# Performance work log

Hardware: AMD Instinct MI355X
Metric: run time of the kernel (lower is better)

The kernel has to match this reference:

```python
import jax, jax.numpy as jnp
import numpy as np

D_MODEL = 1024
NUM_HEADS = 16
EPS = 1e-5


def _layernorm(x, gamma, beta):
    mu = jnp.mean(x, axis=-1, keepdims=True)
    var = jnp.mean(jnp.square(x - mu), axis=-1, keepdims=True)
    return (x - mu) * jax.lax.rsqrt(var + EPS) * gamma + beta


def setup_inputs() -> dict:
    key = jax.random.key(0)
    ks = jax.random.split(key, 8)
    B, S, D = 4, 2048, D_MODEL
    xav = (6.0 / (D + D)) ** 0.5  # xavier_uniform bound for square D x D
    inp = {
        "q": jax.random.normal(ks[0], (B, S, D), dtype=jnp.float32),
        "k": jax.random.normal(ks[1], (B, S, D), dtype=jnp.float32),
        "v": jax.random.normal(ks[2], (B, S, D), dtype=jnp.float32),
        "Wq": jax.random.uniform(ks[3], (D, D), jnp.float32, -xav, xav),
        "Wk": jax.random.uniform(ks[4], (D, D), jnp.float32, -xav, xav),
        "Wv": jax.random.uniform(ks[5], (D, D), jnp.float32, -xav, xav),
        "Wo": jax.random.uniform(ks[6], (D, D), jnp.float32, -xav, xav),
        "bo": jnp.zeros((D,), jnp.float32),
        "q_gamma": jnp.ones((D,), jnp.float32),
        "q_beta": jnp.zeros((D,), jnp.float32),
        "k_gamma": jnp.ones((D,), jnp.float32),
        "k_beta": jnp.zeros((D,), jnp.float32),
    }
    return inp


def reference(q, k, v, Wq, Wk, Wv, Wo, bo, q_gamma, q_beta, k_gamma, k_beta):
    B, S, D = q.shape
    H = NUM_HEADS
    scale = 1.0 / (D ** 0.5)  # NOTE: 1/sqrt(d_model), as in the source
    qp = _layernorm(q @ Wq, q_gamma, q_beta)  # LN over full d_model, pre-split
    kp = _layernorm(k @ Wk, k_gamma, k_beta)
    vp = v @ Wv
    qh = qp.reshape(B, S, H, D // H)  # [B,S,H,hd]
    kh = kp.reshape(B, S, H, D // H)
    vh = vp.reshape(B, S, H, D // H)
    attn = jnp.einsum("bqhd,bkhd->bhqk", qh, kh) * scale
    attn = jax.nn.softmax(attn, axis=-1)
    x = jnp.einsum("bhqk,bkhd->bqhd", attn, vh).reshape(B, S, D)
    return x @ Wo + bo
```

## Files before the change

kernel.cpp:

```cpp
#include <hip/hip_runtime.h>
#include <hip/hip_bf16.h>

typedef unsigned short u16;
typedef __attribute__((ext_vector_type(8))) short bf16x8;
typedef __attribute__((ext_vector_type(4))) float f32x4;
typedef __attribute__((ext_vector_type(16))) float f32x16;
typedef __attribute__((ext_vector_type(4))) unsigned short u16x4;
typedef __attribute__((ext_vector_type(4))) unsigned int u32x4;
typedef __attribute__((ext_vector_type(2))) int i32x2;

__device__ __forceinline__ u16 f2b(float f) {
    __hip_bfloat16 h = __float2bfloat16(f);
    u16 r; __builtin_memcpy(&r, &h, 2); return r;
}
__device__ __forceinline__ float bf2f(u16 u) {
    return __uint_as_float(((unsigned)u) << 16);
}
__device__ __forceinline__ void gload16(const void* g, void* l) {
    __builtin_amdgcn_global_load_lds(
        (const __attribute__((address_space(1))) unsigned int*)g,
        (__attribute__((address_space(3))) unsigned int*)l, 16, 0, 0);
}
__device__ __forceinline__ float fexp2(float x) {
    return __builtin_amdgcn_exp2f(x);
}
__device__ __forceinline__ unsigned cvtpk(float lo, float hi) {
    unsigned d;
    asm("v_cvt_pk_bf16_f32 %0, %1, %2" : "=v"(d) : "v"(lo), "v"(hi));
    return d;
}
__device__ __forceinline__ bf16x8 mk_pa(float a0, float a1, float a2, float a3,
                                        float b0, float b1, float b2, float b3) {
    int A0 = (int)cvtpk(a0, a1), A1 = (int)cvtpk(a2, a3);
    int B0 = (int)cvtpk(b0, b1), B1 = (int)cvtpk(b2, b3);
    i32x2 r0 = __builtin_amdgcn_permlane32_swap(A0, B0, false, false);
    i32x2 r1 = __builtin_amdgcn_permlane32_swap(A1, B1, false, false);
    u32x4 fw = { (unsigned)r0[0], (unsigned)r1[0], (unsigned)r0[1], (unsigned)r1[1] };
    return __builtin_bit_cast(bf16x8, fw);
}

__global__ __launch_bounds__(256)
void wt_kernel(const float* __restrict__ Wq, const float* __restrict__ Wk,
               const float* __restrict__ Wv, const float* __restrict__ Wo,
               u16* __restrict__ Wt) {
    const float* W = blockIdx.z == 0 ? Wq : blockIdx.z == 1 ? Wk : blockIdx.z == 2 ? Wv : Wo;
    u16* Out = Wt + (size_t)blockIdx.z * (1024 * 1024);
    __shared__ float T[64][65];
    const int t = threadIdx.x;
    const int r0 = blockIdx.y * 64, c0 = blockIdx.x * 64;
#pragma unroll
    for (int e = 0; e < 4; ++e) {
        int row = e * 16 + (t >> 4), c4 = (t & 15) * 4;
        f32x4 v = *(const f32x4*)(W + (r0 + row) * 1024 + c0 + c4);
        T[row][c4] = v[0]; T[row][c4 + 1] = v[1]; T[row][c4 + 2] = v[2]; T[row][c4 + 3] = v[3];
    }
    __syncthreads();
#pragma unroll
    for (int e = 0; e < 4; ++e) {
        int orow = e * 16 + (t >> 4), oc4 = (t & 15) * 4;
        u16x4 pk = { f2b(T[oc4][orow]), f2b(T[oc4 + 1][orow]),
                     f2b(T[oc4 + 2][orow]), f2b(T[oc4 + 3][orow]) };
        *(u16x4*)(Out + (c0 + orow) * 1024 + r0 + oc4) = pk;
    }
}

template <int AF32, int BIAS>
__device__ __forceinline__ void gemm_body(const void* __restrict__ Av,
                                          const u16* __restrict__ Bt,
                                          u16* __restrict__ Cb, float* __restrict__ Cf,
                                          const float* __restrict__ bias,
                                          u16* As, u16* Bs, int bx, int by) {
    constexpr int K = 1024;
    const int tid = threadIdx.x;
    const int lane = tid & 63, w = tid >> 6;
    const int wr = w >> 1, wc = w & 1;
    const int c = lane & 15, g = lane >> 4;
    const int m0 = by * 128, n0 = bx * 128;
    const int sr = lane >> 3, sc = (lane & 7) * 8;
    const float* Af = (const float*)Av;
    const u16* Ab = (const u16*)Av;
    f32x4 acc[4][4] = {};
    for (int kt = 0; kt < 16; ++kt) {
        const int k0 = kt * 64;
        if (AF32) {
#pragma unroll
            for (int i = 0; i < 8; ++i) {
                int idx = i * 256 + tid;
                int row = idx >> 4, c4 = (idx & 15) * 4;
                f32x4 v = *(const f32x4*)(Af + (size_t)(m0 + row) * K + k0 + c4);
                u16x4 pk = { f2b(v[0]), f2b(v[1]), f2b(v[2]), f2b(v[3]) };
                *(u16x4*)&As[row * 64 + c4] = pk;
            }
        } else {
#pragma unroll
            for (int i = 0; i < 4; ++i) {
                int row = 32 * w + 8 * i;
                gload16(Ab + (size_t)(m0 + row + sr) * K + k0 + sc, &As[row * 64]);
            }
        }
#pragma unroll
        for (int i = 0; i < 4; ++i) {
            int row = 32 * w + 8 * i;
            gload16(Bt + (size_t)(n0 + row + sr) * K + k0 + sc, &Bs[row * 64]);
        }
        __syncthreads();
#pragma unroll
        for (int kk = 0; kk < 2; ++kk) {
            bf16x8 af[4], bfr[4];
#pragma unroll
            for (int m = 0; m < 4; ++m)
                af[m] = *(const bf16x8*)&As[(wr * 64 + m * 16 + c) * 64 + kk * 32 + 8 * g];
#pragma unroll
            for (int n = 0; n < 4; ++n)
                bfr[n] = *(const bf16x8*)&Bs[(wc * 64 + n * 16 + c) * 64 + kk * 32 + 8 * g];
#pragma unroll
            for (int m = 0; m < 4; ++m)
#pragma unroll
                for (int n = 0; n < 4; ++n)
                    acc[m][n] = __builtin_amdgcn_mfma_f32_16x16x32_bf16(af[m], bfr[n], acc[m][n], 0, 0, 0);
        }
        __syncthreads();
    }
#pragma unroll
    for (int n = 0; n < 4; ++n) {
        int col = n0 + wc * 64 + n * 16 + c;
        float bv = BIAS ? bias[col] : 0.0f;
#pragma unroll
        for (int m = 0; m < 4; ++m) {
            int row0 = m0 + wr * 64 + m * 16 + 4 * g;
#pragma unroll
            for (int r = 0; r < 4; ++r) {
                if (BIAS) Cf[(row0 + r) * 1024 + col] = acc[m][n][r] + bv;
                else      Cb[(row0 + r) * 1024 + col] = f2b(acc[m][n][r]);
            }
        }
    }
}

__global__ __launch_bounds__(256)
void gemm_kernel_f(const u16* __restrict__ Ab, const u16* __restrict__ Bt,
                   float* __restrict__ Cf, const float* __restrict__ bias) {
    __shared__ u16 As[128 * 64];
    __shared__ u16 Bs[128 * 64];
    const int B = blockIdx.x;
    const int bx = (B >> 3) & 7;
    const int by = (B & 7) + 8 * (B >> 6);
    gemm_body<0, 1>(Ab, Bt, nullptr, Cf, bias, As, Bs, bx, by);
}

__global__ __launch_bounds__(256)
void gemm3_kernel(const float* __restrict__ q, const float* __restrict__ k,
                  const float* __restrict__ v, const u16* __restrict__ Wt,
                  u16* __restrict__ C3) {
    __shared__ u16 As[128 * 64];
    __shared__ u16 Bs[128 * 64];
    const int B = blockIdx.x;
    const int bx = (B >> 3) & 7;
    const int p = (B & 7) + 8 * (B >> 6);
    const int by = p & 63;
    const int z = p >> 6;
    const float* Af = z == 0 ? q : z == 1 ? k : v;
    gemm_body<1, 0>((const void*)Af, Wt + (size_t)z * 1048576,
                    C3 + (size_t)z * 8388608, nullptr, nullptr, As, Bs, bx, by);
}

__global__ __launch_bounds__(256)
void gemm1_kernel(const float* __restrict__ Af, const u16* __restrict__ Bt,
                  u16* __restrict__ Cb) {
    __shared__ u16 As[128 * 64];
    __shared__ u16 Bs[128 * 64];
    const int B = blockIdx.x;
    const int bx = (B >> 3) & 7;
    const int by = (B & 7) + 8 * (B >> 6);
    gemm_body<1, 0>((const void*)Af, Bt, Cb, nullptr, nullptr, As, Bs, bx, by);
}

__device__ __forceinline__ void ln_body(const u16* __restrict__ P,
                                        const float* __restrict__ gamma,
                                        const float* __restrict__ beta,
                                        float mul, u16* __restrict__ Out) {
    const int row = blockIdx.x;
    const int tid = threadIdx.x;
    const int lane = tid & 63, w = tid >> 6;
    u16x4 xr = *(const u16x4*)(P + row * 1024 + tid * 4);
    float x0 = bf2f(xr[0]), x1 = bf2f(xr[1]), x2 = bf2f(xr[2]), x3 = bf2f(xr[3]);
    float s = x0 + x1 + x2 + x3;
    float sq = x0 * x0 + x1 * x1 + x2 * x2 + x3 * x3;
#pragma unroll
    for (int m = 1; m < 64; m <<= 1) { s += __shfl_xor(s, m); sq += __shfl_xor(sq, m); }
    __shared__ float red[8];
    if (lane == 0) { red[w] = s; red[4 + w] = sq; }
    __syncthreads();
    float st = red[0] + red[1] + red[2] + red[3];
    float sqt = red[4] + red[5] + red[6] + red[7];
    float mu = st * (1.0f / 1024.0f);
    float var = sqt * (1.0f / 1024.0f) - mu * mu;
    float rs = rsqrtf(var + 1e-5f);
    f32x4 gm = *(const f32x4*)(gamma + tid * 4);
    f32x4 bt = *(const f32x4*)(beta + tid * 4);
    float xs[4] = {x0, x1, x2, x3};
    u16x4 pk;
#pragma unroll
    for (int j = 0; j < 4; ++j)
        pk[j] = f2b(((xs[j] - mu) * rs * gm[j] + bt[j]) * mul);
    const int b = row >> 11, sI = row & 2047;
    const int col = tid * 4, hh = col >> 6, d = col & 63;
    *(u16x4*)(Out + (((b * 16 + hh) * 2048 + sI) << 6) + d) = pk;
}

__global__ __launch_bounds__(256)
void ln_kernel(const u16* __restrict__ P, const float* __restrict__ gamma,
               const float* __restrict__ beta, float mul, u16* __restrict__ Out) {
    ln_body(P, gamma, beta, mul, Out);
}

__global__ __launch_bounds__(256)
void ln2_kernel(const u16* __restrict__ P3,
                const float* __restrict__ qg, const float* __restrict__ qb,
                const float* __restrict__ kg, const float* __restrict__ kb,
                u16* __restrict__ Qa, u16* __restrict__ Ka, float mulq) {
    const int z = blockIdx.z;
    ln_body(P3 + (size_t)z * 8388608, z == 0 ? qg : kg, z == 0 ? qb : kb,
            z == 0 ? mulq : 1.0f, z == 0 ? Qa : Ka);
}

__global__ __launch_bounds__(256)
void vt_kernel(const u16* __restrict__ P, u16* __restrict__ Vt) {
    __shared__ u16 T[64][72];
    const int t = threadIdx.x;
    const int bh = blockIdx.y, s0 = blockIdx.x * 64;
    const int b = bh >> 4, h = bh & 15;
#pragma unroll
    for (int e = 0; e < 4; ++e) {
        int row = e * 16 + (t >> 4), c4 = (t & 15) * 4;
        u16x4 v = *(const u16x4*)(P + (b * 2048 + s0 + row) * 1024 + h * 64 + c4);
        *(u16x4*)&T[row][c4] = v;
    }
    __syncthreads();
#pragma unroll
    for (int e = 0; e < 4; ++e) {
        int dd = e * 16 + (t >> 4), s4 = (t & 15) * 4;
        u16x4 pk = { T[s4][dd], T[s4 + 1][dd], T[s4 + 2][dd], T[s4 + 3][dd] };
        *(u16x4*)(Vt + ((size_t)bh * 64 + dd) * 2048 + s0 + s4) = pk;
    }
}

__global__ __launch_bounds__(256, 4)
void attn_kernel(const u16* __restrict__ Qa, const u16* __restrict__ Ka,
                 const u16* __restrict__ Vt, u16* __restrict__ Xa) {
    __shared__ u16 Ks[2][4096];
    __shared__ u16 Vs[2][4096];
    const int tid = threadIdx.x;
    const int lane = tid & 63, w = tid >> 6;
    const int col = lane & 31, h = lane >> 5;
    const int bid = blockIdx.x;
    const int bh = (bid & 7) * 8 + ((bid >> 3) & 7);
    const int q0 = (bid >> 6) * 128;
    const int b = bh >> 4, hd = bh & 15;
    const int qb = q0 + w * 32;
    const int sw = (col & 7) << 4;

    const u16* qptr = Qa + ((size_t)bh * 2048 + qb + col) * 64;
    bf16x8 qf[4];
#pragma unroll
    for (int s = 0; s < 4; ++s)
        qf[s] = *(const bf16x8*)(qptr + 16 * s + 8 * h);

    const int sr = lane >> 3;
    const int scg = ((lane & 7) ^ sr) * 8;
    const u16* kA = Ka + ((size_t)bh * 2048 + sr) * 64 + scg;
    const u16* vA = Vt + ((size_t)bh * 64 + sr) * 2048 + scg;

    f32x16 o0 = {}, o1 = {};
    float li = 0.f;

#pragma unroll
    for (int j = 0; j < 2; ++j) {
        const int m = 2 * w + j;
        gload16(kA + (size_t)(8 * m) * 64, &Ks[0][8 * m * 64]);
        gload16(vA + (size_t)(8 * m) * 2048, &Vs[0][8 * m * 64]);
    }
    __syncthreads();

    int cur = 0;
    for (int t = 0; t < 32; ++t) {
        const int tn = (t + 1) & 31;
#pragma unroll
        for (int j = 0; j < 2; ++j) {
            const int m = 2 * w + j;
            gload16(kA + (size_t)(tn * 64 + 8 * m) * 64, &Ks[cur ^ 1][8 * m * 64]);
            gload16(vA + (size_t)(8 * m) * 2048 + tn * 64, &Vs[cur ^ 1][8 * m * 64]);
        }

        const char* kbase = (const char*)&Ks[cur][0];
        f32x16 sacc0 = {}, sacc1 = {};
        __builtin_amdgcn_s_setprio(1);
#pragma unroll
        for (int s = 0; s < 4; ++s) {
            bf16x8 kf0 = *(const bf16x8*)(kbase + (col) * 128       + ((32 * s + 16 * h) ^ sw));
            bf16x8 kf1 = *(const bf16x8*)(kbase + (32 + col) * 128  + ((32 * s + 16 * h) ^ sw));
            sacc0 = __builtin_amdgcn_mfma_f32_32x32x16_bf16(kf0, qf[s], sacc0, 0, 0, 0);
            sacc1 = __builtin_amdgcn_mfma_f32_32x32x16_bf16(kf1, qf[s], sacc1, 0, 0, 0);
        }
        __builtin_amdgcn_s_setprio(0);

        f32x16 p0, p1;
#pragma unroll
        for (int r = 0; r < 16; ++r) { p0[r] = fexp2(sacc0[r]); }
#pragma unroll
        for (int r = 0; r < 16; ++r) { p1[r] = fexp2(sacc1[r]); }
#pragma unroll
        for (int r = 0; r < 16; ++r) { li += p0[r] + p1[r]; }

        bf16x8 pa0 = mk_pa(p0[0], p0[1], p0[2], p0[3], p0[4], p0[5], p0[6], p0[7]);
        bf16x8 pa1 = mk_pa(p0[8], p0[9], p0[10], p0[11], p0[12], p0[13], p0[14], p0[15]);
        bf16x8 pa2 = mk_pa(p1[0], p1[1], p1[2], p1[3], p1[4], p1[5], p1[6], p1[7]);
        bf16x8 pa3 = mk_pa(p1[8], p1[9], p1[10], p1[11], p1[12], p1[13], p1[14], p1[15]);

        const char* vb = (const char*)&Vs[cur][0];
        __builtin_amdgcn_s_setprio(1);
#pragma unroll
        for (int sg = 0; sg < 4; ++sg) {
            bf16x8 pf = sg == 0 ? pa0 : sg == 1 ? pa1 : sg == 2 ? pa2 : pa3;
            const int cb = (32 * sg + 16 * h) ^ sw;
            bf16x8 vf0 = *(const bf16x8*)(vb + (col) * 128      + cb);
            bf16x8 vf1 = *(const bf16x8*)(vb + (32 + col) * 128 + cb);
            o0 = __builtin_amdgcn_mfma_f32_32x32x16_bf16(pf, vf0, o0, 0, 0, 0);
            o1 = __builtin_amdgcn_mfma_f32_32x32x16_bf16(pf, vf1, o1, 0, 0, 0);
        }
        __builtin_amdgcn_s_setprio(0);

        __syncthreads();
        cur ^= 1;
    }

    li += __shfl_xor(li, 32);
    float inv = 1.0f / li;
#pragma unroll
    for (int reg = 0; reg < 16; ++reg) {
        const int crow = (reg & 3) + 8 * (reg >> 2) + 4 * h;
        float ivr = __shfl(inv, crow);
        const int row = qb + crow;
        u16* xp = Xa + ((size_t)b * 2048 + row) * 1024 + hd * 64;
        xp[col] = f2b(o0[reg] * ivr);
        xp[32 + col] = f2b(o1[reg] * ivr);
    }
}

extern "C" void kernel_launch(void* const* d_in, const int* in_sizes, int n_in,
                              void* d_out, int out_size, void* d_ws, size_t ws_size,
                              hipStream_t stream) {
    const float* q   = (const float*)d_in[0];
    const float* k   = (const float*)d_in[1];
    const float* v   = (const float*)d_in[2];
    const float* Wq  = (const float*)d_in[3];
    const float* Wk  = (const float*)d_in[4];
    const float* Wv  = (const float*)d_in[5];
    const float* Wo  = (const float*)d_in[6];
    const float* bo  = (const float*)d_in[7];
    const float* qg  = (const float*)d_in[8];
    const float* qbt = (const float*)d_in[9];
    const float* kg  = (const float*)d_in[10];
    const float* kbt = (const float*)d_in[11];

    char* ws = (char*)d_ws;
    const float MUL_Q = 0.04508422002778f;

    if (ws_size >= 109051904ULL) {
        u16* Wt  = (u16*)(ws);
        u16* Qa  = (u16*)(ws + 8388608);
        u16* Ka  = (u16*)(ws + 25165824);
        u16* Vt  = (u16*)(ws + 41943040);
        u16* Pb3 = (u16*)(ws + 58720256);
        u16* Xa  = Pb3;

        wt_kernel<<<dim3(16, 16, 4), 256, 0, stream>>>(Wq, Wk, Wv, Wo, Wt);
        gemm3_kernel<<<1536, 256, 0, stream>>>(q, k, v, Wt, Pb3);
        ln2_kernel<<<dim3(8192, 1, 2), 256, 0, stream>>>(Pb3, qg, qbt, kg, kbt, Qa, Ka, MUL_Q);
        vt_kernel<<<dim3(32, 64), 256, 0, stream>>>(Pb3 + 2 * 8388608, Vt);
        attn_kernel<<<1024, 256, 0, stream>>>(Qa, Ka, Vt, Xa);
        gemm_kernel_f<<<512, 256, 0, stream>>>((const u16*)Xa, Wt + 3145728, (float*)d_out, bo);
    } else {
        u16* Wt = (u16*)(ws);
        u16* Pb = (u16*)(ws + 8388608);
        u16* Qa = (u16*)(ws + 25165824);
        u16* Ka = (u16*)(ws + 41943040);
        u16* Vt = (u16*)(ws + 58720256);
        u16* Xa = Pb;

        wt_kernel<<<dim3(16, 16, 4), 256, 0, stream>>>(Wq, Wk, Wv, Wo, Wt);
        gemm1_kernel<<<512, 256, 0, stream>>>(q, Wt, Pb);
        ln_kernel<<<8192, 256, 0, stream>>>(Pb, qg, qbt, MUL_Q, Qa);
        gemm1_kernel<<<512, 256, 0, stream>>>(k, Wt + 1048576, Pb);
        ln_kernel<<<8192, 256, 0, stream>>>(Pb, kg, kbt, 1.0f, Ka);
        gemm1_kernel<<<512, 256, 0, stream>>>(v, Wt + 2097152, Pb);
        vt_kernel<<<dim3(32, 64), 256, 0, stream>>>(Pb, Vt);
        attn_kernel<<<1024, 256, 0, stream>>>(Qa, Ka, Vt, Xa);
        gemm_kernel_f<<<512, 256, 0, stream>>>((const u16*)Xa, Wt + 3145728, (float*)d_out, bo);
    }
}
```

Before: 234.4 us.

## Prefetch fp32 A tiles into registers two steps ahead in projection GEMM

Adds a dedicated fp32-input GEMM body that loads the next-next A tile into registers while the current tile is consumed by MFMAs, then converts and stores to LDS after the barrier. The goal is to hide global load latency of fp32 activations that previously stalled each k-step. It costs 32 extra VGPRs for the register staging, which may reduce occupancy. The bf16 path is simplified to a single template parameter.

```diff
diff --git a/kernel.cpp b/kernel.cpp
--- a/kernel.cpp
+++ b/kernel.cpp
@@ -64,8 +64,8 @@
     }
 }
 
-template <int AF32, int BIAS>
-__device__ __forceinline__ void gemm_body(const void* __restrict__ Av,
+template <int BIAS>
+__device__ __forceinline__ void gemm_body(const u16* __restrict__ Ab,
                                           const u16* __restrict__ Bt,
                                           u16* __restrict__ Cb, float* __restrict__ Cf,
                                           const float* __restrict__ bias,
@@ -77,30 +77,13 @@
     const int c = lane & 15, g = lane >> 4;
     const int m0 = by * 128, n0 = bx * 128;
     const int sr = lane >> 3, sc = (lane & 7) * 8;
-    const float* Af = (const float*)Av;
-    const u16* Ab = (const u16*)Av;
     f32x4 acc[4][4] = {};
     for (int kt = 0; kt < 16; ++kt) {
         const int k0 = kt * 64;
-        if (AF32) {
-#pragma unroll
-            for (int i = 0; i < 8; ++i) {
-                int idx = i * 256 + tid;
-                int row = idx >> 4, c4 = (idx & 15) * 4;
-                f32x4 v = *(const f32x4*)(Af + (size_t)(m0 + row) * K + k0 + c4);
-                u16x4 pk = { f2b(v[0]), f2b(v[1]), f2b(v[2]), f2b(v[3]) };
-                *(u16x4*)&As[row * 64 + c4] = pk;
-            }
-        } else {
-#pragma unroll
-            for (int i = 0; i < 4; ++i) {
-                int row = 32 * w + 8 * i;
-                gload16(Ab + (size_t)(m0 + row + sr) * K + k0 + sc, &As[row * 64]);
-            }
-        }
 #pragma unroll
         for (int i = 0; i < 4; ++i) {
             int row = 32 * w + 8 * i;
+            gload16(Ab + (size_t)(m0 + row + sr) * K + k0 + sc, &As[row * 64]);
             gload16(Bt + (size_t)(n0 + row + sr) * K + k0 + sc, &Bs[row * 64]);
         }
         __syncthreads();
@@ -133,6 +116,91 @@
                 if (BIAS) Cf[(row0 + r) * 1024 + col] = acc[m][n][r] + bv;
                 else      Cb[(row0 + r) * 1024 + col] = f2b(acc[m][n][r]);
             }
+        }
+    }
+}
+
+__device__ __forceinline__ void gemm_body_f32(const float* __restrict__ Af,
+                                              const u16* __restrict__ Bt,
+                                              u16* __restrict__ Cb,
+                                              u16* As, u16* Bs, int bx, int by) {
+    constexpr int K = 1024;
+    const int tid = threadIdx.x;
+    const int lane = tid & 63, w = tid >> 6;
+    const int wr = w >> 1, wc = w & 1;
+    const int c = lane & 15, g = lane >> 4;
+    const int m0 = by * 128, n0 = bx * 128;
+    const int sr = lane >> 3, sc = (lane & 7) * 8;
+    const int arow = tid >> 4, ac4 = (tid & 15) * 4;
+    const float* aBase = Af + (size_t)(m0 + arow) * K + ac4;
+    f32x4 acc[4][4] = {};
+    f32x4 areg[8];
+
+#pragma unroll
+    for (int i = 0; i < 8; ++i)
+        areg[i] = *(const f32x4*)(aBase + (size_t)(16 * i) * K);
+#pragma unroll
+    for (int i = 0; i < 8; ++i) {
+        u16x4 pk = { f2b(areg[i][0]), f2b(areg[i][1]), f2b(areg[i][2]), f2b(areg[i][3]) };
+        *(u16x4*)&As[(arow + 16 * i) * 64 + ac4] = pk;
+    }
+#pragma unroll
+    for (int i = 0; i < 4; ++i) {
+        int row = 32 * w + 8 * i;
+        gload16(Bt + (size_t)(n0 + row + sr) * K + sc, &Bs[row * 64]);
+    }
+#pragma unroll
+    for (int i = 0; i < 8; ++i)
+        areg[i] = *(const f32x4*)(aBase + (size_t)(16 * i) * K + 64);
+    __syncthreads();
+
+    for (int kt = 0; kt < 16; ++kt) {
+#pragma unroll
+        for (int kk = 0; kk < 2; ++kk) {
+            bf16x8 af[4], bfr[4];
+#pragma unroll
+            for (int m = 0; m < 4; ++m)
+                af[m] = *(const bf16x8*)&As[(wr * 64 + m * 16 + c) * 64 + kk * 32 + 8 * g];
+#pragma unroll
+            for (int n = 0; n < 4; ++n)
+                bfr[n] = *(const bf16x8*)&Bs[(wc * 64 + n * 16 + c) * 64 + kk * 32 + 8 * g];
+#pragma unroll
+            for (int m = 0; m < 4; ++m)
+#pragma unroll
+                for (int n = 0; n < 4; ++n)
+                    acc[m][n] = __builtin_amdgcn_mfma_f32_16x16x32_bf16(af[m], bfr[n], acc[m][n], 0, 0, 0);
+        }
+        __syncthreads();
+        if (kt < 15) {
+#pragma unroll
+            for (int i = 0; i < 8; ++i) {
+                u16x4 pk = { f2b(areg[i][0]), f2b(areg[i][1]), f2b(areg[i][2]), f2b(areg[i][3]) };
+                *(u16x4*)&As[(arow + 16 * i) * 64 + ac4] = pk;
+            }
+            const int k1 = (kt + 1) * 64;
+#pragma unroll
+            for (int i = 0; i < 4; ++i) {
+                int row = 32 * w + 8 * i;
+                gload16(Bt + (size_t)(n0 + row + sr) * K + k1 + sc, &Bs[row * 64]);
+            }
+            if (kt < 14) {
+                const int k2 = (kt + 2) * 64;
+#pragma unroll
+                for (int i = 0; i < 8; ++i)
+                    areg[i] = *(const f32x4*)(aBase + (size_t)(16 * i) * K + k2);
+            }
+            __syncthreads();
+        }
+    }
+#pragma unroll
+    for (int n = 0; n < 4; ++n) {
+        int col = n0 + wc * 64 + n * 16 + c;
+#pragma unroll
+        for (int m = 0; m < 4; ++m) {
+            int row0 = m0 + wr * 64 + m * 16 + 4 * g;
+#pragma unroll
+            for (int r = 0; r < 4; ++r)
+                Cb[(row0 + r) * 1024 + col] = f2b(acc[m][n][r]);
         }
     }
 }
@@ -145,7 +213,7 @@
     const int B = blockIdx.x;
     const int bx = (B >> 3) & 7;
     const int by = (B & 7) + 8 * (B >> 6);
-    gemm_body<0, 1>(Ab, Bt, nullptr, Cf, bias, As, Bs, bx, by);
+    gemm_body<1>(Ab, Bt, nullptr, Cf, bias, As, Bs, bx, by);
 }
 
 __global__ __launch_bounds__(256)
@@ -160,8 +228,8 @@
     const int by = p & 63;
     const int z = p >> 6;
     const float* Af = z == 0 ? q : z == 1 ? k : v;
-    gemm_body<1, 0>((const void*)Af, Wt + (size_t)z * 1048576,
-                    C3 + (size_t)z * 8388608, nullptr, nullptr, As, Bs, bx, by);
+    gemm_body_f32(Af, Wt + (size_t)z * 1048576,
+                  C3 + (size_t)z * 8388608, As, Bs, bx, by);
 }
 
 __global__ __launch_bounds__(256)
@@ -172,7 +240,7 @@
     const int B = blockIdx.x;
     const int bx = (B >> 3) & 7;
     const int by = (B & 7) + 8 * (B >> 6);
-    gemm_body<1, 0>((const void*)Af, Bt, Cb, nullptr, nullptr, As, Bs, bx, by);
+    gemm_body_f32(Af, Bt, Cb, As, Bs, bx, by);
 }
 
 __device__ __forceinline__ void ln_body(const u16* __restrict__ P,
```

Result: slower. 243.0 us (+3.7%).

## Fuse V transpose into LN launch and compute softmax row sums via MFMA

Applied to the files above, without the earlier changes.

The V transpose is merged into the LayerNorm launch as a third z-slice, with extra blocks exiting early, which removes one kernel launch. In the attention kernel the per-lane exp sum and final shuffles are replaced by an extra MFMA against a ones vector, so row sums come out directly in the accumulator layout. This trades scalar adds and shuffles for one more MFMA per step plus 16 more accumulator registers. It also changes the sum to use the bf16-rounded probabilities, which matches the numerator.

```diff
diff --git a/kernel.cpp b/kernel.cpp
--- a/kernel.cpp
+++ b/kernel.cpp
@@ -214,21 +214,11 @@
     ln_body(P, gamma, beta, mul, Out);
 }
 
-__global__ __launch_bounds__(256)
-void ln2_kernel(const u16* __restrict__ P3,
-                const float* __restrict__ qg, const float* __restrict__ qb,
-                const float* __restrict__ kg, const float* __restrict__ kb,
-                u16* __restrict__ Qa, u16* __restrict__ Ka, float mulq) {
-    const int z = blockIdx.z;
-    ln_body(P3 + (size_t)z * 8388608, z == 0 ? qg : kg, z == 0 ? qb : kb,
-            z == 0 ? mulq : 1.0f, z == 0 ? Qa : Ka);
-}
-
-__global__ __launch_bounds__(256)
-void vt_kernel(const u16* __restrict__ P, u16* __restrict__ Vt) {
+__device__ __forceinline__ void vt_body(const u16* __restrict__ P, u16* __restrict__ Vt,
+                                        int sblk, int bh) {
     __shared__ u16 T[64][72];
     const int t = threadIdx.x;
-    const int bh = blockIdx.y, s0 = blockIdx.x * 64;
+    const int s0 = sblk * 64;
     const int b = bh >> 4, h = bh & 15;
 #pragma unroll
     for (int e = 0; e < 4; ++e) {
@@ -242,6 +232,28 @@
         int dd = e * 16 + (t >> 4), s4 = (t & 15) * 4;
         u16x4 pk = { T[s4][dd], T[s4 + 1][dd], T[s4 + 2][dd], T[s4 + 3][dd] };
         *(u16x4*)(Vt + ((size_t)bh * 64 + dd) * 2048 + s0 + s4) = pk;
+    }
+}
+
+__global__ __launch_bounds__(256)
+void vt_kernel(const u16* __restrict__ P, u16* __restrict__ Vt) {
+    vt_body(P, Vt, blockIdx.x, blockIdx.y);
+}
+
+__global__ __launch_bounds__(256)
+void lnvt_kernel(const u16* __restrict__ P3,
+                 const float* __restrict__ qg, const float* __restrict__ qb,
+                 const float* __restrict__ kg, const float* __restrict__ kb,
+                 u16* __restrict__ Qa, u16* __restrict__ Ka,
+                 u16* __restrict__ Vt, float mulq) {
+    const int z = blockIdx.z;
+    if (z < 2) {
+        ln_body(P3 + (size_t)z * 8388608, z == 0 ? qg : kg, z == 0 ? qb : kb,
+                z == 0 ? mulq : 1.0f, z == 0 ? Qa : Ka);
+    } else {
+        const int bid = blockIdx.x;
+        if (bid >= 2048) return;
+        vt_body(P3 + 2 * 8388608, Vt, bid & 31, bid >> 5);
     }
 }
 
@@ -271,8 +283,11 @@
     const u16* kA = Ka + ((size_t)bh * 2048 + sr) * 64 + scg;
     const u16* vA = Vt + ((size_t)bh * 64 + sr) * 2048 + scg;
 
-    f32x16 o0 = {}, o1 = {};
-    float li = 0.f;
+    bf16x8 vones;
+#pragma unroll
+    for (int j = 0; j < 8; ++j) vones[j] = (short)0x3F80;
+
+    f32x16 o0 = {}, o1 = {}, o2 = {};
 
 #pragma unroll
     for (int j = 0; j < 2; ++j) {
@@ -309,8 +324,6 @@
         for (int r = 0; r < 16; ++r) { p0[r] = fexp2(sacc0[r]); }
 #pragma unroll
         for (int r = 0; r < 16; ++r) { p1[r] = fexp2(sacc1[r]); }
-#pragma unroll
-        for (int r = 0; r < 16; ++r) { li += p0[r] + p1[r]; }
 
         bf16x8 pa0 = mk_pa(p0[0], p0[1], p0[2], p0[3], p0[4], p0[5], p0[6], p0[7]);
         bf16x8 pa1 = mk_pa(p0[8], p0[9], p0[10], p0[11], p0[12], p0[13], p0[14], p0[15]);
@@ -327,6 +340,7 @@
             bf16x8 vf1 = *(const bf16x8*)(vb + (32 + col) * 128 + cb);
             o0 = __builtin_amdgcn_mfma_f32_32x32x16_bf16(pf, vf0, o0, 0, 0, 0);
             o1 = __builtin_amdgcn_mfma_f32_32x32x16_bf16(pf, vf1, o1, 0, 0, 0);
+            o2 = __builtin_amdgcn_mfma_f32_32x32x16_bf16(pf, vones, o2, 0, 0, 0);
         }
         __builtin_amdgcn_s_setprio(0);
 
@@ -334,12 +348,10 @@
         cur ^= 1;
     }
 
-    li += __shfl_xor(li, 32);
-    float inv = 1.0f / li;
 #pragma unroll
     for (int reg = 0; reg < 16; ++reg) {
         const int crow = (reg & 3) + 8 * (reg >> 2) + 4 * h;
-        float ivr = __shfl(inv, crow);
+        float ivr = 1.0f / o2[reg];
         const int row = qb + crow;
         u16* xp = Xa + ((size_t)b * 2048 + row) * 1024 + hd * 64;
         xp[col] = f2b(o0[reg] * ivr);
@@ -376,8 +388,7 @@
 
         wt_kernel<<<dim3(16, 16, 4), 256, 0, stream>>>(Wq, Wk, Wv, Wo, Wt);
         gemm3_kernel<<<1536, 256, 0, stream>>>(q, k, v, Wt, Pb3);
-        ln2_kernel<<<dim3(8192, 1, 2), 256, 0, stream>>>(Pb3, qg, qbt, kg, kbt, Qa, Ka, MUL_Q);
-        vt_kernel<<<dim3(32, 64), 256, 0, stream>>>(Pb3 + 2 * 8388608, Vt);
+        lnvt_kernel<<<dim3(8192, 1, 3), 256, 0, stream>>>(Pb3, qg, qbt, kg, kbt, Qa, Ka, Vt, MUL_Q);
         attn_kernel<<<1024, 256, 0, stream>>>(Qa, Ka, Vt, Xa);
         gemm_kernel_f<<<512, 256, 0, stream>>>((const u16*)Xa, Wt + 3145728, (float*)d_out, bo);
     } else {
```

Measured after the change: 253.4 us. +8.1%, slower.

## Widen fused QKV projection GEMM tile to 128x256 with inline body

Applied to the files above, without the earlier changes.

The fused QKV projection GEMM now uses a custom inline body with a 128x256 output tile per block instead of the shared 128x128 gemm_body, which halves the block count to 768. Each wave computes a 64x128 sub-tile with 4x8 MFMA accumulators. This means the fp32 activation rows are loaded and converted to bf16 half as often across the N dimension, cutting global traffic on the large fp32 inputs. In exchange it uses far more accumulator registers and a larger LDS B tile, and the loop has no double buffering, so occupancy and latency hiding may suffer.

```diff
diff --git a/kernel.cpp b/kernel.cpp
--- a/kernel.cpp
+++ b/kernel.cpp
@@ -152,16 +152,69 @@
 void gemm3_kernel(const float* __restrict__ q, const float* __restrict__ k,
                   const float* __restrict__ v, const u16* __restrict__ Wt,
                   u16* __restrict__ C3) {
+    constexpr int K = 1024;
     __shared__ u16 As[128 * 64];
-    __shared__ u16 Bs[128 * 64];
+    __shared__ u16 Bs[256 * 64];
     const int B = blockIdx.x;
-    const int bx = (B >> 3) & 7;
-    const int p = (B & 7) + 8 * (B >> 6);
+    const int bx = (B >> 3) & 3;
+    const int p = (B & 7) + 8 * (B >> 5);
     const int by = p & 63;
     const int z = p >> 6;
     const float* Af = z == 0 ? q : z == 1 ? k : v;
-    gemm_body<1, 0>((const void*)Af, Wt + (size_t)z * 1048576,
-                    C3 + (size_t)z * 8388608, nullptr, nullptr, As, Bs, bx, by);
+    const u16* Bt = Wt + (size_t)z * 1048576;
+    u16* Cb = C3 + (size_t)z * 8388608;
+
+    const int tid = threadIdx.x;
+    const int lane = tid & 63, w = tid >> 6;
+    const int wr = w >> 1, wc = w & 1;
+    const int c = lane & 15, g = lane >> 4;
+    const int m0 = by * 128, n0 = bx * 256;
+    const int sr = lane >> 3, sc = (lane & 7) * 8;
+    f32x4 acc[4][8] = {};
+    for (int kt = 0; kt < 16; ++kt) {
+        const int k0 = kt * 64;
+#pragma unroll
+        for (int i = 0; i < 8; ++i) {
+            int idx = i * 256 + tid;
+            int row = idx >> 4, c4 = (idx & 15) * 4;
+            f32x4 vv = *(const f32x4*)(Af + (size_t)(m0 + row) * K + k0 + c4);
+            u16x4 pk = { f2b(vv[0]), f2b(vv[1]), f2b(vv[2]), f2b(vv[3]) };
+            *(u16x4*)&As[row * 64 + c4] = pk;
+        }
+#pragma unroll
+        for (int i = 0; i < 8; ++i) {
+            int m = w * 8 + i;
+            gload16(Bt + (size_t)(n0 + 8 * m + sr) * K + k0 + sc, &Bs[8 * m * 64]);
+        }
+        __syncthreads();
+#pragma unroll
+        for (int kk = 0; kk < 2; ++kk) {
+            bf16x8 af[4], bfr[8];
+#pragma unroll
+            for (int m = 0; m < 4; ++m)
+                af[m] = *(const bf16x8*)&As[(wr * 64 + m * 16 + c) * 64 + kk * 32 + 8 * g];
+#pragma unroll
+            for (int n = 0; n < 8; ++n)
+                bfr[n] = *(const bf16x8*)&Bs[(wc * 128 + n * 16 + c) * 64 + kk * 32 + 8 * g];
+#pragma unroll
+            for (int m = 0; m < 4; ++m)
+#pragma unroll
+                for (int n = 0; n < 8; ++n)
+                    acc[m][n] = __builtin_amdgcn_mfma_f32_16x16x32_bf16(af[m], bfr[n], acc[m][n], 0, 0, 0);
+        }
+        __syncthreads();
+    }
+#pragma unroll
+    for (int n = 0; n < 8; ++n) {
+        int col = n0 + wc * 128 + n * 16 + c;
+#pragma unroll
+        for (int m = 0; m < 4; ++m) {
+            int row0 = m0 + wr * 64 + m * 16 + 4 * g;
+#pragma unroll
+            for (int r = 0; r < 4; ++r)
+                Cb[(row0 + r) * 1024 + col] = f2b(acc[m][n][r]);
+        }
+    }
 }
 
 __global__ __launch_bounds__(256)
@@ -375,7 +428,7 @@
         u16* Xa  = Pb3;
 
         wt_kernel<<<dim3(16, 16, 4), 256, 0, stream>>>(Wq, Wk, Wv, Wo, Wt);
-        gemm3_kernel<<<1536, 256, 0, stream>>>(q, k, v, Wt, Pb3);
+        gemm3_kernel<<<768, 256, 0, stream>>>(q, k, v, Wt, Pb3);
         ln2_kernel<<<dim3(8192, 1, 2), 256, 0, stream>>>(Pb3, qg, qbt, kg, kbt, Qa, Ka, MUL_Q);
         vt_kernel<<<dim3(32, 64), 256, 0, stream>>>(Pb3 + 2 * 8388608, Vt);
         attn_kernel<<<1024, 256, 0, stream>>>(Qa, Ka, Vt, Xa);
```

Result: slower. 265.5 us (+13.3%).
